# Kernel optimization log

Measured on AMD Instinct MI355X. Metric: run time of the kernel, lower is better.

Reference implementation:

```python
import jax, jax.numpy as jnp
import numpy as np

B, T, SEG = 64, 16, 50          # batch, n segments, segment length (cap 50 in original)
E, D, H, F = 512, 512, 8, 2048  # dim_embeddings, dim_encoder, n_heads, dim_ff
DH = D // H
SCALE = float(1.0 / np.sqrt(DH))


def _ln(x, g, b):
    m = jnp.mean(x, -1, keepdims=True)
    v = jnp.var(x, -1, keepdims=True)
    return (x - m) * jax.lax.rsqrt(v + 1e-5) * g + b


def _mha(q_in, kv_in, Wq, Wk, Wv, Wo, kv_lens):
    b, sq, _ = q_in.shape
    sk = kv_in.shape[1]
    q = (q_in @ Wq).reshape(b, sq, H, DH)
    k = (kv_in @ Wk).reshape(b, sk, H, DH)
    v = (kv_in @ Wv).reshape(b, sk, H, DH)
    scores = jnp.einsum('bqhd,bkhd->bhqk', q, k) * SCALE
    mask = jnp.arange(sk)[None, :] < kv_lens[:, None]  # [b, sk] key-padding mask
    scores = jnp.where(mask[:, None, None, :], scores, -1e9)
    a = jax.nn.softmax(scores, axis=-1)
    o = jnp.einsum('bhqk,bkhd->bqhd', a, v).reshape(b, sq, D)
    return o @ Wo


def _ffn(x, W1, W2):
    return jax.nn.relu(x @ W1) @ W2


def _encoder(x, lens, p):
    # TransformerEncoder: project E->D, masked self-attn + FFN, post-LN residuals
    h = x @ p['eWin']
    h = _ln(h + _mha(h, h, p['eWq'], p['eWk'], p['eWv'], p['eWo'], lens), p['eG1'], p['eB1'])
    return _ln(h + _ffn(h, p['eF1'], p['eF2']), p['eG2'], p['eB2'])


def _connection(prev, curr, prev_lens, p):
    # Connection: curr cross-attends over prev (masked by prev_lens) + FFN
    h = _ln(curr + _mha(curr, prev, p['cWq'], p['cWk'], p['cWv'], p['cWo'], prev_lens), p['cG1'], p['cB1'])
    return _ln(h + _ffn(h, p['cF1'], p['cF2']), p['cG2'], p['cB2'])


def _forward(seqs, ends, p):
    first_lens = jnp.minimum(ends[:, 0], SEG)
    encoded = _encoder(seqs[:, :SEG], first_lens, p)  # [B, SEG, D]
    # regular segmentation: ends[b,t] = (t+1)*SEG, so every step uses a full segment
    segs = seqs.reshape(B, T, SEG, E).transpose(1, 0, 2, 3)[1:]        # [T-1, B, SEG, E]
    seg_lens = jnp.minimum(ends[:, 1:] - ends[:, :-1], SEG).T          # [T-1, B]
    prev_lens = jnp.full((B,), SEG, jnp.int32)

    def step(enc, xs):
        seg, lens = xs
        currs = _encoder(seg, lens, p)
        out = _connection(enc, currs, prev_lens, p)
        return out, None  # out[-SEG:] == out since seq_len = min(diff, 50) = SEG

    encoded, _ = jax.lax.scan(step, encoded, (segs, seg_lens))
    return encoded


def setup_inputs():
    key = jax.random.key(0)
    ks = jax.random.split(key, 16)
    g = lambda k, s: jax.random.normal(k, s, jnp.float32) * 0.02
    inp = {
        'seqs': jax.random.normal(ks[0], (B, T * SEG, E), jnp.float32),
        'ends': jnp.broadcast_to((jnp.arange(1, T + 1) * SEG).astype(jnp.int32), (B, T)),
        'eWin': g(ks[1], (E, D)),
        'eWq': g(ks[2], (D, D)), 'eWk': g(ks[3], (D, D)),
        'eWv': g(ks[4], (D, D)), 'eWo': g(ks[5], (D, D)),
        'eG1': jnp.ones(D), 'eB1': jnp.zeros(D),
        'eF1': g(ks[6], (D, F)), 'eF2': g(ks[7], (F, D)),
        'eG2': jnp.ones(D), 'eB2': jnp.zeros(D),
        'cWq': g(ks[8], (D, D)), 'cWk': g(ks[9], (D, D)),
        'cWv': g(ks[10], (D, D)), 'cWo': g(ks[11], (D, D)),
        'cG1': jnp.ones(D), 'cB1': jnp.zeros(D),
        'cF1': g(ks[12], (D, F)), 'cF2': g(ks[13], (F, D)),
        'cG2': jnp.ones(D), 'cB2': jnp.zeros(D),
    }
    return inp


def reference(seqs, ends, eWin, eWq, eWk, eWv, eWo, eG1, eB1, eF1, eF2, eG2, eB2,
              cWq, cWk, cWv, cWo, cG1, cB1, cF1, cF2, cG2, cB2):
    p = dict(eWin=eWin, eWq=eWq, eWk=eWk, eWv=eWv, eWo=eWo, eG1=eG1, eB1=eB1,
             eF1=eF1, eF2=eF2, eG2=eG2, eB2=eB2, cWq=cWq, cWk=cWk, cWv=cWv,
             cWo=cWo, cG1=cG1, cB1=cB1, cF1=cF1, cF2=cF2, cG2=cG2, cB2=cB2)
    return _forward(seqs, ends, p)
```

## Files before the change

### kernel.cpp

```cpp
#include <hip/hip_runtime.h>


#define NB   64
#define NT   16
#define SEGL 50
#define DMODEL 512
#define DFF  2048
#define NHEAD 8
#define DHEAD 64

typedef unsigned short ushort_t;
typedef __attribute__((ext_vector_type(8))) short bfrag;
typedef __attribute__((ext_vector_type(4))) float ffrag;

__device__ __forceinline__ ushort_t f2b(float x) {
    union { float f; unsigned u; } c; c.f = x;
    unsigned r = c.u + 0x7fffu + ((c.u >> 16) & 1u);
    return (ushort_t)(r >> 16);
}

#define GLOAD_LDS16(g, l) __builtin_amdgcn_global_load_lds( \
    (const __attribute__((address_space(1))) void*)(g),      \
    (__attribute__((address_space(3))) void*)(l), 16, 0, 0)

template<int BM, int BN, int WROWS, int WCOLS>
__global__ __launch_bounds__(256) void mfma_gemm(
    const ushort_t* __restrict__ A, int agrp, long long astride,
    const ushort_t* __restrict__ Bt, ushort_t* __restrict__ C,
    int M, int N, int K, int relu)
{
    constexpr int WM = BM / WROWS, WN = BN / WCOLS;
    constexpr int SM = WM / 16, SN = WN / 16;
    constexpr int NSUBA = BM / 16, NSUBB = BN / 16;
    constexpr int NSUB = NSUBA + NSUBB;
    constexpr int NINST = NSUB * 2;
    constexpr int IPW = NINST / 4;
    constexpr int BUFS = NSUB * 1024;
    constexpr int EST = WN + 8;
    constexpr int LDS_KLOOP = 2 * BUFS;
    constexpr int LDS_EPI   = 4 * WM * EST;
    constexpr int LDS_SZ = LDS_KLOOP > LDS_EPI ? LDS_KLOOP : LDS_EPI;
    __shared__ ushort_t lds[LDS_SZ];

    const int tid = threadIdx.x;
    const int wave = tid >> 6, lane = tid & 63;
    const int wrow = wave / WCOLS, wcol = wave % WCOLS;
    const int bm = blockIdx.y * BM, bn = blockIdx.x * BN;
    const int lm = lane & 15, lq = lane >> 4;

    ffrag acc[SM][SN];
#pragma unroll
    for (int i = 0; i < SM; ++i)
#pragma unroll
        for (int j = 0; j < SN; ++j) acc[i][j] = (ffrag){0.f, 0.f, 0.f, 0.f};

    const ushort_t* gptr[IPW];
    int loff[IPW];
#pragma unroll
    for (int e = 0; e < IPW; ++e) {
        int g = wave * IPW + e;
        int s = g >> 1, h = g & 1;
        if (s < NSUBA) {
            int m = bm + s * 16 + lm;
            gptr[e] = A + (long long)(m / agrp) * astride
                        + (long long)(m % agrp) * K + h * 32 + lq * 8;
        } else {
            int n = bn + (s - NSUBA) * 16 + lm;
            gptr[e] = Bt + (long long)n * K + h * 32 + lq * 8;
        }
        loff[e] = s * 1024 + h * 512;
    }

#pragma unroll
    for (int e = 0; e < IPW; ++e)
        GLOAD_LDS16(gptr[e], &lds[loff[e]]);

    const int nk = K >> 6;
    for (int kk = 0; kk < nk; ++kk) {
        __syncthreads();
        if (kk + 1 < nk) {
            const int koff = (kk + 1) << 6;
            const int nb = (kk + 1) & 1;
#pragma unroll
            for (int e = 0; e < IPW; ++e)
                GLOAD_LDS16(gptr[e] + koff, &lds[nb * BUFS + loff[e]]);
        }
        const ushort_t* lb = &lds[(kk & 1) * BUFS];
#pragma unroll
        for (int h = 0; h < 2; ++h) {
            bfrag af[SM], bfg[SN];
#pragma unroll
            for (int i = 0; i < SM; ++i)
                af[i] = *(const bfrag*)&lb[(wrow * SM + i) * 1024 + h * 512 + lane * 8];
#pragma unroll
            for (int j = 0; j < SN; ++j)
                bfg[j] = *(const bfrag*)&lb[(NSUBA + wcol * SN + j) * 1024 + h * 512 + lane * 8];
#pragma unroll
            for (int i = 0; i < SM; ++i)
#pragma unroll
                for (int j = 0; j < SN; ++j)
                    acc[i][j] = __builtin_amdgcn_mfma_f32_16x16x32_bf16(
                        af[i], bfg[j], acc[i][j], 0, 0, 0);
        }
    }

    __syncthreads();
    ushort_t* ep = &lds[wave * WM * EST];
#pragma unroll
    for (int i = 0; i < SM; ++i)
#pragma unroll
        for (int j = 0; j < SN; ++j)
#pragma unroll
            for (int r = 0; r < 4; ++r) {
                int row = i * 16 + lq * 4 + r;
                int col = j * 16 + lm;
                float v = acc[i][j][r];
                if (relu) v = fmaxf(v, 0.f);
                ep[row * EST + col] = f2b(v);
            }
    constexpr int CPR = WN / 8;
    constexpr int RPI = 64 / CPR;
    const int lrow = lane / CPR, lcol = (lane % CPR) * 8;
#pragma unroll
    for (int it = 0; it < WM / RPI; ++it) {
        int row = it * RPI + lrow;
        uint4 v = *(const uint4*)&ep[row * EST + lcol];
        long long grow = bm + wrow * WM + row;
        int gcol = bn + wcol * WN + lcol;
        *(uint4*)&C[grow * N + gcol] = v;
    }
}

__global__ __launch_bounds__(256) void wtrans_k(
    const float* __restrict__ W, ushort_t* __restrict__ Wt, int K, int N)
{
    __shared__ float t[32][33];
    const int bk = blockIdx.y * 32, bn = blockIdx.x * 32;
    const int tx = threadIdx.x & 31, ty = threadIdx.x >> 5;
    for (int i = ty; i < 32; i += 8)
        t[i][tx] = W[(long long)(bk + i) * N + bn + tx];
    __syncthreads();
    for (int i = ty; i < 32; i += 8)
        Wt[(long long)(bn + i) * K + bk + tx] = f2b(t[tx][i]);
}

__global__ __launch_bounds__(256) void cvt_k(
    const float* __restrict__ in, ushort_t* __restrict__ out, long long n)
{
    long long i = ((long long)blockIdx.x * 256 + threadIdx.x) * 8;
    if (i >= n) return;
    float4 a = *(const float4*)(in + i);
    float4 b = *(const float4*)(in + i + 4);
    ushort_t o[8] = {f2b(a.x), f2b(a.y), f2b(a.z), f2b(a.w),
                     f2b(b.x), f2b(b.y), f2b(b.z), f2b(b.w)};
    *(uint4*)(out + i) = *(const uint4*)o;
}

__global__ __launch_bounds__(256) void attn_mfma_k(
    const ushort_t* __restrict__ Q, long long qns, long long qrs,
    const ushort_t* __restrict__ K, const ushort_t* __restrict__ V,
    long long kns, long long kvrs,
    ushort_t* __restrict__ O,
    const int* __restrict__ lens, int G, int t0)
{
    __shared__ ushort_t qs[64][72];
    __shared__ ushort_t ks[64][72];
    __shared__ ushort_t vt[64][72];
    const int n = blockIdx.x >> 3, h = blockIdx.x & 7;
    const int tid = threadIdx.x;
    const int wave = tid >> 6, lane = tid & 63;
    const int lm = lane & 15, lq = lane >> 4;
    int len = SEGL;
    if (lens) {
        int b = n / G, t = t0 + (n % G);
        len = lens[b * NT + t];
        if (len > SEGL) len = SEGL;
    }
    {
        uint4 z = {0, 0, 0, 0};
        uint4* vz = (uint4*)&vt[0][0];
        for (int i = tid; i < 64 * 72 / 8; i += 256) vz[i] = z;
    }
    __syncthreads();
    for (int idx = tid; idx < SEGL * 8; idx += 256) {
        int s = idx >> 3, d8 = (idx & 7) << 3;
        const ushort_t* qp = Q + (long long)n * qns + (long long)s * qrs + h * DHEAD + d8;
        const ushort_t* kp = K + (long long)n * kns + (long long)s * kvrs + h * DHEAD + d8;
        const ushort_t* vp = V + (long long)n * kns + (long long)s * kvrs + h * DHEAD + d8;
        *(uint4*)&qs[s][d8] = *(const uint4*)qp;
        *(uint4*)&ks[s][d8] = *(const uint4*)kp;
        uint4 v4 = *(const uint4*)vp;
        const ushort_t* vv = (const ushort_t*)&v4;
#pragma unroll
        for (int u = 0; u < 8; ++u) vt[d8 + u][s] = vv[u];
    }
    __syncthreads();

    ffrag sc[4];
#pragma unroll
    for (int nt = 0; nt < 4; ++nt) sc[nt] = (ffrag){0.f, 0.f, 0.f, 0.f};
#pragma unroll
    for (int kt = 0; kt < 2; ++kt) {
        bfrag a = *(const bfrag*)&qs[wave * 16 + lm][kt * 32 + lq * 8];
#pragma unroll
        for (int nt = 0; nt < 4; ++nt) {
            bfrag b = *(const bfrag*)&ks[nt * 16 + lm][kt * 32 + lq * 8];
            sc[nt] = __builtin_amdgcn_mfma_f32_16x16x32_bf16(a, b, sc[nt], 0, 0, 0);
        }
    }
    __syncthreads();

#pragma unroll
    for (int r = 0; r < 4; ++r) {
        float x[4];
        float mx = -1e30f;
#pragma unroll
        for (int nt = 0; nt < 4; ++nt) {
            int col = nt * 16 + lm;
            x[nt] = (col < len) ? sc[nt][r] * 0.125f : -1e9f;
            mx = fmaxf(mx, x[nt]);
        }
        for (int off = 8; off; off >>= 1) mx = fmaxf(mx, __shfl_xor(mx, off));
        float e[4], se = 0.f;
#pragma unroll
        for (int nt = 0; nt < 4; ++nt) { e[nt] = __expf(x[nt] - mx); se += e[nt]; }
        for (int off = 8; off; off >>= 1) se += __shfl_xor(se, off);
        float inv = 1.f / se;
        int row = wave * 16 + lq * 4 + r;
#pragma unroll
        for (int nt = 0; nt < 4; ++nt)
            qs[row][nt * 16 + lm] = f2b(e[nt] * inv);
    }
    __syncthreads();

    ffrag oc[4];
#pragma unroll
    for (int dt = 0; dt < 4; ++dt) oc[dt] = (ffrag){0.f, 0.f, 0.f, 0.f};
#pragma unroll
    for (int kt = 0; kt < 2; ++kt) {
        bfrag a = *(const bfrag*)&qs[wave * 16 + lm][kt * 32 + lq * 8];
#pragma unroll
        for (int dt = 0; dt < 4; ++dt) {
            bfrag b = *(const bfrag*)&vt[dt * 16 + lm][kt * 32 + lq * 8];
            oc[dt] = __builtin_amdgcn_mfma_f32_16x16x32_bf16(a, b, oc[dt], 0, 0, 0);
        }
    }
#pragma unroll
    for (int r = 0; r < 4; ++r) {
        int i = wave * 16 + lq * 4 + r;
        if (i < SEGL) {
            ushort_t* op = O + (long long)(n * SEGL + i) * DMODEL + h * DHEAD + lm;
#pragma unroll
            for (int dt = 0; dt < 4; ++dt)
                op[dt * 16] = f2b(oc[dt][r]);
        }
    }
}

__global__ __launch_bounds__(256) void cross_attn_k(
    const ushort_t* __restrict__ Qp, long long qns, long long qrs,
    const ushort_t* __restrict__ Prev, int pgrp, long long pstride,
    const ushort_t* __restrict__ Wkv,
    ushort_t* __restrict__ O)
{
    __shared__ ushort_t xp[64 * 264];
    __shared__ ushort_t qs[64][72];
    const int n = blockIdx.x >> 3, h = blockIdx.x & 7;
    const int tid = threadIdx.x;
    const int wave = tid >> 6, lane = tid & 63;
    const int lm = lane & 15, lq = lane >> 4;

    for (int idx = tid; idx < SEGL * 8; idx += 256) {
        int s = idx >> 3, d8 = (idx & 7) << 3;
        *(uint4*)&qs[s][d8] =
            *(const uint4*)(Qp + (long long)n * qns + (long long)s * qrs + h * DHEAD + d8);
    }

    const ushort_t* wbase = Wkv +
        (long long)((wave >> 1) * 512 + h * 64 + (wave & 1) * 32) * 512;
    ffrag kv[4][2];
#pragma unroll
    for (int i = 0; i < 4; ++i)
#pragma unroll
        for (int j = 0; j < 2; ++j) kv[i][j] = (ffrag){0.f, 0.f, 0.f, 0.f};

#pragma unroll
    for (int half = 0; half < 2; ++half) {
        __syncthreads();
        for (int idx = tid; idx < 64 * 33; idx += 256) {
            int s = idx / 33, c8 = (idx % 33) * 8;
            uint4 v = {0, 0, 0, 0};
            if (s < SEGL && c8 < 256) {
                long long r = (long long)n * SEGL + s;
                v = *(const uint4*)(Prev + (r / pgrp) * pstride
                                    + (r % pgrp) * DMODEL + half * 256 + c8);
            }
            *(uint4*)&xp[s * 264 + c8] = v;
        }
        __syncthreads();
#pragma unroll
        for (int k8 = 0; k8 < 8; ++k8) {
            const int kg = half * 256 + k8 * 32;
            bfrag bf[2], af[4];
#pragma unroll
            for (int j = 0; j < 2; ++j)
                bf[j] = *(const bfrag*)(wbase + (long long)(j * 16 + lm) * 512 + kg + lq * 8);
#pragma unroll
            for (int i = 0; i < 4; ++i)
                af[i] = *(const bfrag*)&xp[(i * 16 + lm) * 264 + k8 * 32 + lq * 8];
#pragma unroll
            for (int i = 0; i < 4; ++i)
#pragma unroll
                for (int j = 0; j < 2; ++j)
                    kv[i][j] = __builtin_amdgcn_mfma_f32_16x16x32_bf16(
                        af[i], bf[j], kv[i][j], 0, 0, 0);
        }
    }
    __syncthreads();
    ushort_t (*ks)[72] = (ushort_t(*)[72])&xp[0];
    ushort_t (*vt)[72] = (ushort_t(*)[72])&xp[64 * 72];
#pragma unroll
    for (int i = 0; i < 4; ++i)
#pragma unroll
        for (int j = 0; j < 2; ++j)
#pragma unroll
            for (int r = 0; r < 4; ++r) {
                int rowk = i * 16 + lq * 4 + r;
                int d = (wave & 1) * 32 + j * 16 + lm;
                ushort_t val = f2b(kv[i][j][r]);
                if (wave < 2) ks[rowk][d] = val;
                else          vt[d][rowk] = val;
            }
    __syncthreads();

    ffrag sc[4];
#pragma unroll
    for (int nt = 0; nt < 4; ++nt) sc[nt] = (ffrag){0.f, 0.f, 0.f, 0.f};
#pragma unroll
    for (int kt = 0; kt < 2; ++kt) {
        bfrag a = *(const bfrag*)&qs[wave * 16 + lm][kt * 32 + lq * 8];
#pragma unroll
        for (int nt = 0; nt < 4; ++nt) {
            bfrag b = *(const bfrag*)&ks[nt * 16 + lm][kt * 32 + lq * 8];
            sc[nt] = __builtin_amdgcn_mfma_f32_16x16x32_bf16(a, b, sc[nt], 0, 0, 0);
        }
    }
    __syncthreads();

#pragma unroll
    for (int r = 0; r < 4; ++r) {
        float x[4];
        float mx = -1e30f;
#pragma unroll
        for (int nt = 0; nt < 4; ++nt) {
            int col = nt * 16 + lm;
            x[nt] = (col < SEGL) ? sc[nt][r] * 0.125f : -1e9f;
            mx = fmaxf(mx, x[nt]);
        }
        for (int off = 8; off; off >>= 1) mx = fmaxf(mx, __shfl_xor(mx, off));
        float e[4], se = 0.f;
#pragma unroll
        for (int nt = 0; nt < 4; ++nt) { e[nt] = __expf(x[nt] - mx); se += e[nt]; }
        for (int off = 8; off; off >>= 1) se += __shfl_xor(se, off);
        float inv = 1.f / se;
        int row = wave * 16 + lq * 4 + r;
#pragma unroll
        for (int nt = 0; nt < 4; ++nt)
            qs[row][nt * 16 + lm] = f2b(e[nt] * inv);
    }
    __syncthreads();

    ffrag oc[4];
#pragma unroll
    for (int dt = 0; dt < 4; ++dt) oc[dt] = (ffrag){0.f, 0.f, 0.f, 0.f};
#pragma unroll
    for (int kt = 0; kt < 2; ++kt) {
        bfrag a = *(const bfrag*)&qs[wave * 16 + lm][kt * 32 + lq * 8];
#pragma unroll
        for (int dt = 0; dt < 4; ++dt) {
            bfrag b = *(const bfrag*)&vt[dt * 16 + lm][kt * 32 + lq * 8];
            oc[dt] = __builtin_amdgcn_mfma_f32_16x16x32_bf16(a, b, oc[dt], 0, 0, 0);
        }
    }
#pragma unroll
    for (int r = 0; r < 4; ++r) {
        int i = wave * 16 + lq * 4 + r;
        if (i < SEGL) {
            ushort_t* op = O + (long long)(n * SEGL + i) * DMODEL + h * DHEAD + lm;
#pragma unroll
            for (int dt = 0; dt < 4; ++dt)
                op[dt * 16] = f2b(oc[dt][r]);
        }
    }
}

template<bool OUTF32>
__global__ __launch_bounds__(256) void add_ln_k(
    const ushort_t* __restrict__ A, int agrp, long long astride,
    const ushort_t* __restrict__ Bv,
    const float* __restrict__ gamma, const float* __restrict__ beta,
    void* __restrict__ O, int ogrp, long long ostride, int M)
{
    const int wave = threadIdx.x >> 6, lane = threadIdx.x & 63;
    const int r = blockIdx.x * 4 + wave;
    if (r >= M) return;
    const ushort_t* a = A + (long long)(r / agrp) * astride + (long long)(r % agrp) * DMODEL;
    const ushort_t* b = Bv + (long long)r * DMODEL;
    float x[8];
    {
        uint4 a4 = *(const uint4*)(a + lane * 8);
        uint4 b4 = *(const uint4*)(b + lane * 8);
        const unsigned* aa = (const unsigned*)&a4;
        const unsigned* bb = (const unsigned*)&b4;
#pragma unroll
        for (int c = 0; c < 4; ++c) {
            union { unsigned u; float f; } alo, ahi, blo, bhi;
            alo.u = aa[c] << 16; ahi.u = aa[c] & 0xffff0000u;
            blo.u = bb[c] << 16; bhi.u = bb[c] & 0xffff0000u;
            x[2 * c]     = alo.f + blo.f;
            x[2 * c + 1] = ahi.f + bhi.f;
        }
    }
    float s = 0.f, s2 = 0.f;
#pragma unroll
    for (int i = 0; i < 8; ++i) { s += x[i]; s2 = fmaf(x[i], x[i], s2); }
    for (int off = 32; off; off >>= 1) {
        s += __shfl_xor(s, off);
        s2 += __shfl_xor(s2, off);
    }
    const float mean = s * (1.f / DMODEL);
    const float var = s2 * (1.f / DMODEL) - mean * mean;
    const float inv = rsqrtf(var + 1e-5f);
    float4 g0 = *(const float4*)(gamma + lane * 8);
    float4 g1 = *(const float4*)(gamma + lane * 8 + 4);
    float4 be0 = *(const float4*)(beta + lane * 8);
    float4 be1 = *(const float4*)(beta + lane * 8 + 4);
    float y[8];
    y[0] = (x[0] - mean) * inv * g0.x + be0.x;
    y[1] = (x[1] - mean) * inv * g0.y + be0.y;
    y[2] = (x[2] - mean) * inv * g0.z + be0.z;
    y[3] = (x[3] - mean) * inv * g0.w + be0.w;
    y[4] = (x[4] - mean) * inv * g1.x + be1.x;
    y[5] = (x[5] - mean) * inv * g1.y + be1.y;
    y[6] = (x[6] - mean) * inv * g1.z + be1.z;
    y[7] = (x[7] - mean) * inv * g1.w + be1.w;
    if (OUTF32) {
        float* o = (float*)O + (long long)(r / ogrp) * ostride + (long long)(r % ogrp) * DMODEL;
        *(float4*)(o + lane * 8) = *(float4*)&y[0];
        *(float4*)(o + lane * 8 + 4) = *(float4*)&y[4];
    } else {
        ushort_t* o = (ushort_t*)O + (long long)(r / ogrp) * ostride + (long long)(r % ogrp) * DMODEL;
        ushort_t ob[8];
#pragma unroll
        for (int i = 0; i < 8; ++i) ob[i] = f2b(y[i]);
        *(uint4*)(o + lane * 8) = *(const uint4*)ob;
    }
}

__global__ void lens_k(const int* __restrict__ ends, int* __restrict__ lens)
{
    int i = blockIdx.x * 256 + threadIdx.x;
    if (i >= NB * NT) return;
    int t = i & (NT - 1);
    int prev = t ? ends[i - 1] : 0;
    int l = ends[i] - prev;
    if (l > SEGL) l = SEGL;
    lens[i] = l;
}

extern "C" void kernel_launch(void* const* d_in, const int* in_sizes, int n_in,
                              void* d_out, int out_size, void* d_ws, size_t ws_size,
                              hipStream_t stream)
{
    const float* seqs = (const float*)d_in[0];
    const int*   ends = (const int*)d_in[1];
    const float* eG1 = (const float*)d_in[7],  *eB1 = (const float*)d_in[8];
    const float* eG2 = (const float*)d_in[11], *eB2 = (const float*)d_in[12];
    const float* cG1 = (const float*)d_in[17], *cB1 = (const float*)d_in[18];
    const float* cG2 = (const float*)d_in[21], *cB2 = (const float*)d_in[22];
    float* out = (float*)d_out;

    const int G = (ws_size >= (size_t)470000000) ? 8 : 4;
    const long long CH = 1638400LL * G;

    ushort_t* ws = (ushort_t*)d_ws;
    const long long SEQROW = (long long)NT * SEGL * DMODEL;
    ushort_t* SEQB = ws;
    ushort_t* WT   = SEQB + 26214400LL;
    ushort_t* ENC  = WT   + 6553600LL;
    ushort_t* BUF0 = ENC  + 26214400LL;
    ushort_t* QKV  = BUF0 + CH;
    ushort_t* BUF4 = QKV  + 3 * CH;
    ushort_t* BUF1 = BUF4 + CH;
    ushort_t* BUF2 = BUF1 + CH;
    ushort_t* MID  = BUF2 + CH;
    ushort_t* OUTB = MID  + 4 * CH;
    ushort_t* QALL = OUTB + 1638400LL;
    int*      lens = (int*)(QALL + 24576000LL);

    const ushort_t* eWinT = WT + 0;
    const ushort_t* WQKVe = WT + 262144;
    const ushort_t* eWoT  = WT + 1048576;
    const ushort_t* eF1T  = WT + 1310720;
    const ushort_t* eF2T  = WT + 2359296;
    const ushort_t* cWqT  = WT + 3407872;
    const ushort_t* cKV   = WT + 3670016;
    const ushort_t* cWoT  = WT + 4194304;
    const ushort_t* cF1T  = WT + 4456448;
    const ushort_t* cF2T  = WT + 5505024;

    struct WMap { int src; long long dst; int K, N; };
    const WMap wm[13] = {
        {2,  0,       512, 512},
        {3,  262144,  512, 512},
        {4,  524288,  512, 512},
        {5,  786432,  512, 512},
        {6,  1048576, 512, 512},
        {9,  1310720, 512, 2048},
        {10, 2359296, 2048, 512},
        {13, 3407872, 512, 512},
        {14, 3670016, 512, 512},
        {15, 3932160, 512, 512},
        {16, 4194304, 512, 512},
        {19, 4456448, 512, 2048},
        {20, 5505024, 2048, 512},
    };

    cvt_k<<<12800, 256, 0, stream>>>(seqs, SEQB, 26214400LL);
    for (int w = 0; w < 13; ++w) {
        dim3 g(wm[w].N / 32, wm[w].K / 32);
        wtrans_k<<<g, 256, 0, stream>>>((const float*)d_in[wm[w].src],
                                        WT + wm[w].dst, wm[w].K, wm[w].N);
    }
    lens_k<<<4, 256, 0, stream>>>(ends, lens);

    auto gemmL = [&](const ushort_t* A, int agrp, long long astr, const ushort_t* Bt,
                     ushort_t* C, int M, int N, int K, int relu) {
        dim3 g(N / 128, M / 128);
        mfma_gemm<128, 128, 2, 2><<<g, 256, 0, stream>>>(A, agrp, astr, Bt, C, M, N, K, relu);
    };
    auto gemmS = [&](const ushort_t* A, int agrp, long long astr, const ushort_t* Bt,
                     ushort_t* C, int M, int N, int K, int relu) {
        dim3 g(N / 64, M / 64);
        mfma_gemm<64, 64, 2, 2><<<g, 256, 0, stream>>>(A, agrp, astr, Bt, C, M, N, K, relu);
    };

    const int Mc = NB * G * SEGL;
    for (int c = 0; c < NT / G; ++c) {
        const int t0 = c * G;
        const ushort_t* Abase = SEQB + (long long)t0 * SEGL * DMODEL;
        ushort_t* ENCc = ENC + (long long)t0 * SEGL * DMODEL;
        gemmL(Abase, G * SEGL, SEQROW, eWinT, BUF0, Mc, 512, 512, 0);
        gemmL(BUF0, Mc, 0, WQKVe, QKV, Mc, 1536, 512, 0);
        attn_mfma_k<<<NB * G * NHEAD, 256, 0, stream>>>(
            QKV, 50LL * 1536, 1536, QKV + 512, QKV + 1024, 50LL * 1536, 1536,
            BUF4, lens, G, t0);
        gemmL(BUF4, Mc, 0, eWoT, BUF1, Mc, 512, 512, 0);
        add_ln_k<false><<<Mc / 4, 256, 0, stream>>>(BUF0, Mc, 0, BUF1, eG1, eB1,
                                                    BUF2, Mc, 0, Mc);
        gemmL(BUF2, Mc, 0, eF1T, MID, Mc, 2048, 512, 1);
        gemmL(MID, Mc, 0, eF2T, BUF1, Mc, 512, 2048, 0);
        add_ln_k<false><<<Mc / 4, 256, 0, stream>>>(BUF2, Mc, 0, BUF1, eG2, eB2,
                                                    ENCc, G * SEGL, SEQROW, Mc);
    }

    gemmL(ENC + 25600, 750, SEQROW, cWqT, QALL, 48000, 512, 512, 0);

    const int Ms = NB * SEGL;
    for (int t = 1; t < NT; ++t) {
        const ushort_t* currA = ENC + (long long)t * SEGL * DMODEL;
        const ushort_t* prevA; int pg; long long ps;
        if (t == 1) { prevA = ENC;  pg = SEGL; ps = SEQROW; }
        else        { prevA = OUTB; pg = Ms;   ps = 0; }
        cross_attn_k<<<NB * NHEAD, 256, 0, stream>>>(
            QALL + (long long)(t - 1) * 25600, 750LL * 512, 512,
            prevA, pg, ps, cKV, BUF4);
        gemmS(BUF4, Ms, 0, cWoT, BUF0, Ms, 512, 512, 0);
        add_ln_k<false><<<Ms / 4, 256, 0, stream>>>(currA, SEGL, SEQROW, BUF0, cG1, cB1,
                                                    BUF2, Ms, 0, Ms);
        gemmS(BUF2, Ms, 0, cF1T, MID, Ms, 2048, 512, 1);
        gemmS(MID, Ms, 0, cF2T, BUF0, Ms, 512, 2048, 0);
        if (t == NT - 1)
            add_ln_k<true><<<Ms / 4, 256, 0, stream>>>(BUF2, Ms, 0, BUF0, cG2, cB2,
                                                       out, Ms, 0, Ms);
        else
            add_ln_k<false><<<Ms / 4, 256, 0, stream>>>(BUF2, Ms, 0, BUF0, cG2, cB2,
                                                        OUTB, Ms, 0, Ms);
    }
}
```

Before: 2.770 ms.

## Fuse sequential cross-attention phase into one persistent per-batch kernel

Replaces the 15-step host loop of cross_attn/Wo GEMM/LN/FFN GEMMs/LN launches with a single persistent kernel, phase2_seq. It launches 64 blocks of 1024 threads, one per batch element, and each block loops over all timesteps with the previous output kept in LDS and intermediates in a per-block global scratch. The aim is to remove roughly 100 small kernel launches and the inter-kernel round trips. In exchange it uses only 64 workgroups on a GPU with many more CUs, and each block recomputes K/V and streams all the weights from L2 on every step, so compute parallelism is low.

```diff
diff --git a/kernel.cpp b/kernel.cpp
--- a/kernel.cpp
+++ b/kernel.cpp
@@ -22,6 +22,8 @@
 #define GLOAD_LDS16(g, l) __builtin_amdgcn_global_load_lds( \
     (const __attribute__((address_space(1))) void*)(g),      \
     (__attribute__((address_space(3))) void*)(l), 16, 0, 0)
+
+#define MFMA16(a, b, c) __builtin_amdgcn_mfma_f32_16x16x32_bf16(a, b, c, 0, 0, 0)
 
 template<int BM, int BN, int WROWS, int WCOLS>
 __global__ __launch_bounds__(256) void mfma_gemm(
@@ -99,8 +101,7 @@
             for (int i = 0; i < SM; ++i)
 #pragma unroll
                 for (int j = 0; j < SN; ++j)
-                    acc[i][j] = __builtin_amdgcn_mfma_f32_16x16x32_bf16(
-                        af[i], bfg[j], acc[i][j], 0, 0, 0);
+                    acc[i][j] = MFMA16(af[i], bfg[j], acc[i][j]);
         }
     }
 
@@ -205,7 +206,7 @@
 #pragma unroll
         for (int nt = 0; nt < 4; ++nt) {
             bfrag b = *(const bfrag*)&ks[nt * 16 + lm][kt * 32 + lq * 8];
-            sc[nt] = __builtin_amdgcn_mfma_f32_16x16x32_bf16(a, b, sc[nt], 0, 0, 0);
+            sc[nt] = MFMA16(a, b, sc[nt]);
         }
     }
     __syncthreads();
@@ -242,144 +243,7 @@
 #pragma unroll
         for (int dt = 0; dt < 4; ++dt) {
             bfrag b = *(const bfrag*)&vt[dt * 16 + lm][kt * 32 + lq * 8];
-            oc[dt] = __builtin_amdgcn_mfma_f32_16x16x32_bf16(a, b, oc[dt], 0, 0, 0);
-        }
-    }
-#pragma unroll
-    for (int r = 0; r < 4; ++r) {
-        int i = wave * 16 + lq * 4 + r;
-        if (i < SEGL) {
-            ushort_t* op = O + (long long)(n * SEGL + i) * DMODEL + h * DHEAD + lm;
-#pragma unroll
-            for (int dt = 0; dt < 4; ++dt)
-                op[dt * 16] = f2b(oc[dt][r]);
-        }
-    }
-}
-
-__global__ __launch_bounds__(256) void cross_attn_k(
-    const ushort_t* __restrict__ Qp, long long qns, long long qrs,
-    const ushort_t* __restrict__ Prev, int pgrp, long long pstride,
-    const ushort_t* __restrict__ Wkv,
-    ushort_t* __restrict__ O)
-{
-    __shared__ ushort_t xp[64 * 264];
-    __shared__ ushort_t qs[64][72];
-    const int n = blockIdx.x >> 3, h = blockIdx.x & 7;
-    const int tid = threadIdx.x;
-    const int wave = tid >> 6, lane = tid & 63;
-    const int lm = lane & 15, lq = lane >> 4;
-
-    for (int idx = tid; idx < SEGL * 8; idx += 256) {
-        int s = idx >> 3, d8 = (idx & 7) << 3;
-        *(uint4*)&qs[s][d8] =
-            *(const uint4*)(Qp + (long long)n * qns + (long long)s * qrs + h * DHEAD + d8);
-    }
-
-    const ushort_t* wbase = Wkv +
-        (long long)((wave >> 1) * 512 + h * 64 + (wave & 1) * 32) * 512;
-    ffrag kv[4][2];
-#pragma unroll
-    for (int i = 0; i < 4; ++i)
-#pragma unroll
-        for (int j = 0; j < 2; ++j) kv[i][j] = (ffrag){0.f, 0.f, 0.f, 0.f};
-
-#pragma unroll
-    for (int half = 0; half < 2; ++half) {
-        __syncthreads();
-        for (int idx = tid; idx < 64 * 33; idx += 256) {
-            int s = idx / 33, c8 = (idx % 33) * 8;
-            uint4 v = {0, 0, 0, 0};
-            if (s < SEGL && c8 < 256) {
-                long long r = (long long)n * SEGL + s;
-                v = *(const uint4*)(Prev + (r / pgrp) * pstride
-                                    + (r % pgrp) * DMODEL + half * 256 + c8);
-            }
-            *(uint4*)&xp[s * 264 + c8] = v;
-        }
-        __syncthreads();
-#pragma unroll
-        for (int k8 = 0; k8 < 8; ++k8) {
-            const int kg = half * 256 + k8 * 32;
-            bfrag bf[2], af[4];
-#pragma unroll
-            for (int j = 0; j < 2; ++j)
-                bf[j] = *(const bfrag*)(wbase + (long long)(j * 16 + lm) * 512 + kg + lq * 8);
-#pragma unroll
-            for (int i = 0; i < 4; ++i)
-                af[i] = *(const bfrag*)&xp[(i * 16 + lm) * 264 + k8 * 32 + lq * 8];
-#pragma unroll
-            for (int i = 0; i < 4; ++i)
-#pragma unroll
-                for (int j = 0; j < 2; ++j)
-                    kv[i][j] = __builtin_amdgcn_mfma_f32_16x16x32_bf16(
-                        af[i], bf[j], kv[i][j], 0, 0, 0);
-        }
-    }
-    __syncthreads();
-    ushort_t (*ks)[72] = (ushort_t(*)[72])&xp[0];
-    ushort_t (*vt)[72] = (ushort_t(*)[72])&xp[64 * 72];
-#pragma unroll
-    for (int i = 0; i < 4; ++i)
-#pragma unroll
-        for (int j = 0; j < 2; ++j)
-#pragma unroll
-            for (int r = 0; r < 4; ++r) {
-                int rowk = i * 16 + lq * 4 + r;
-                int d = (wave & 1) * 32 + j * 16 + lm;
-                ushort_t val = f2b(kv[i][j][r]);
-                if (wave < 2) ks[rowk][d] = val;
-                else          vt[d][rowk] = val;
-            }
-    __syncthreads();
-
-    ffrag sc[4];
-#pragma unroll
-    for (int nt = 0; nt < 4; ++nt) sc[nt] = (ffrag){0.f, 0.f, 0.f, 0.f};
-#pragma unroll
-    for (int kt = 0; kt < 2; ++kt) {
-        bfrag a = *(const bfrag*)&qs[wave * 16 + lm][kt * 32 + lq * 8];
-#pragma unroll
-        for (int nt = 0; nt < 4; ++nt) {
-            bfrag b = *(const bfrag*)&ks[nt * 16 + lm][kt * 32 + lq * 8];
-            sc[nt] = __builtin_amdgcn_mfma_f32_16x16x32_bf16(a, b, sc[nt], 0, 0, 0);
-        }
-    }
-    __syncthreads();
-
-#pragma unroll
-    for (int r = 0; r < 4; ++r) {
-        float x[4];
-        float mx = -1e30f;
-#pragma unroll
-        for (int nt = 0; nt < 4; ++nt) {
-            int col = nt * 16 + lm;
-            x[nt] = (col < SEGL) ? sc[nt][r] * 0.125f : -1e9f;
-            mx = fmaxf(mx, x[nt]);
-        }
-        for (int off = 8; off; off >>= 1) mx = fmaxf(mx, __shfl_xor(mx, off));
-        float e[4], se = 0.f;
-#pragma unroll
-        for (int nt = 0; nt < 4; ++nt) { e[nt] = __expf(x[nt] - mx); se += e[nt]; }
-        for (int off = 8; off; off >>= 1) se += __shfl_xor(se, off);
-        float inv = 1.f / se;
-        int row = wave * 16 + lq * 4 + r;
-#pragma unroll
-        for (int nt = 0; nt < 4; ++nt)
-            qs[row][nt * 16 + lm] = f2b(e[nt] * inv);
-    }
-    __syncthreads();
-
-    ffrag oc[4];
-#pragma unroll
-    for (int dt = 0; dt < 4; ++dt) oc[dt] = (ffrag){0.f, 0.f, 0.f, 0.f};
-#pragma unroll
-    for (int kt = 0; kt < 2; ++kt) {
-        bfrag a = *(const bfrag*)&qs[wave * 16 + lm][kt * 32 + lq * 8];
-#pragma unroll
-        for (int dt = 0; dt < 4; ++dt) {
-            bfrag b = *(const bfrag*)&vt[dt * 16 + lm][kt * 32 + lq * 8];
-            oc[dt] = __builtin_amdgcn_mfma_f32_16x16x32_bf16(a, b, oc[dt], 0, 0, 0);
+            oc[dt] = MFMA16(a, b, oc[dt]);
         }
     }
 #pragma unroll
@@ -468,6 +332,338 @@
     lens[i] = l;
 }
 
+__global__ __launch_bounds__(1024) void phase2_seq(
+    const ushort_t* __restrict__ ENC, const ushort_t* __restrict__ QALL,
+    const ushort_t* __restrict__ Wkv, const ushort_t* __restrict__ WoT,
+    const ushort_t* __restrict__ F1T, const ushort_t* __restrict__ F2T,
+    const float* __restrict__ G1v, const float* __restrict__ B1v,
+    const float* __restrict__ G2v, const float* __restrict__ B2v,
+    ushort_t* __restrict__ SCR, float* __restrict__ out)
+{
+    extern __shared__ ushort_t lds[];
+    ushort_t* Pb = lds;
+    ushort_t* Mb = lds + 64 * 520;
+    const int n = blockIdx.x;
+    const int tid = threadIdx.x;
+    const int w = tid >> 6, lane = tid & 63;
+    const int lm = lane & 15, lq = lane >> 4;
+    const int hh = w >> 1, wp = w & 1;
+
+    ushort_t* Kg  = SCR + (long long)n * 163840;
+    ushort_t* VTg = Kg + 32768;
+    ushort_t* Sg  = Kg + 65536;
+    ushort_t* ATg = Kg + 98304;
+    ushort_t* Hg  = Kg + 131072;
+
+    {
+        uint4 z = {0, 0, 0, 0};
+        for (int i = tid; i < 64 * 520 / 8; i += 1024) ((uint4*)Pb)[i] = z;
+    }
+    __syncthreads();
+    for (int idx = tid; idx < 50 * 64; idx += 1024) {
+        int s = idx >> 6, c8 = (idx & 63) << 3;
+        *(uint4*)&Pb[s * 520 + c8] =
+            *(const uint4*)(ENC + (long long)n * 409600 + (long long)s * 512 + c8);
+    }
+    __syncthreads();
+
+#pragma unroll 1
+    for (int t = 1; t < NT; ++t) {
+        const ushort_t* Qb = QALL + (long long)n * 384000 + (long long)(t - 1) * 25600;
+
+        {
+            ffrag ka[4][2], va[4][2];
+#pragma unroll
+            for (int i = 0; i < 4; ++i)
+#pragma unroll
+                for (int j = 0; j < 2; ++j) {
+                    ka[i][j] = (ffrag){0.f, 0.f, 0.f, 0.f};
+                    va[i][j] = (ffrag){0.f, 0.f, 0.f, 0.f};
+                }
+            const ushort_t* wk = Wkv + (long long)(w * 32) * 512;
+            const ushort_t* wv = Wkv + (long long)(512 + w * 32) * 512;
+#pragma unroll
+            for (int k8 = 0; k8 < 16; ++k8) {
+                bfrag af[4];
+#pragma unroll
+                for (int i = 0; i < 4; ++i)
+                    af[i] = *(const bfrag*)&Pb[(i * 16 + lm) * 520 + k8 * 32 + lq * 8];
+#pragma unroll
+                for (int j = 0; j < 2; ++j) {
+                    bfrag bk = *(const bfrag*)(wk + (long long)(j * 16 + lm) * 512 + k8 * 32 + lq * 8);
+                    bfrag bv = *(const bfrag*)(wv + (long long)(j * 16 + lm) * 512 + k8 * 32 + lq * 8);
+#pragma unroll
+                    for (int i = 0; i < 4; ++i) {
+                        ka[i][j] = MFMA16(af[i], bk, ka[i][j]);
+                        va[i][j] = MFMA16(af[i], bv, va[i][j]);
+                    }
+                }
+            }
+#pragma unroll
+            for (int i = 0; i < 4; ++i)
+#pragma unroll
+                for (int j = 0; j < 2; ++j)
+#pragma unroll
+                    for (int r = 0; r < 4; ++r) {
+                        int row = i * 16 + lq * 4 + r;
+                        int col = w * 32 + j * 16 + lm;
+                        Kg[row * 512 + col] = f2b(ka[i][j][r]);
+                        VTg[col * 64 + row] = f2b(va[i][j][r]);
+                    }
+        }
+        __syncthreads();
+
+        {
+            ffrag sc[2][4];
+#pragma unroll
+            for (int i = 0; i < 2; ++i)
+#pragma unroll
+                for (int j = 0; j < 4; ++j) sc[i][j] = (ffrag){0.f, 0.f, 0.f, 0.f};
+#pragma unroll
+            for (int kk = 0; kk < 2; ++kk) {
+                bfrag aq[2];
+#pragma unroll
+                for (int ii = 0; ii < 2; ++ii)
+                    aq[ii] = *(const bfrag*)(Qb + (long long)((wp * 2 + ii) * 16 + lm) * 512
+                                             + hh * 64 + kk * 32 + lq * 8);
+#pragma unroll
+                for (int j = 0; j < 4; ++j) {
+                    bfrag bk = *(const bfrag*)&Kg[(j * 16 + lm) * 512 + hh * 64 + kk * 32 + lq * 8];
+#pragma unroll
+                    for (int ii = 0; ii < 2; ++ii)
+                        sc[ii][j] = MFMA16(aq[ii], bk, sc[ii][j]);
+                }
+            }
+#pragma unroll
+            for (int ii = 0; ii < 2; ++ii)
+#pragma unroll
+                for (int r = 0; r < 4; ++r) {
+                    float x[4], mx = -1e30f;
+#pragma unroll
+                    for (int j = 0; j < 4; ++j) {
+                        int col = j * 16 + lm;
+                        x[j] = (col < SEGL) ? sc[ii][j][r] * 0.125f : -1e9f;
+                        mx = fmaxf(mx, x[j]);
+                    }
+                    for (int off = 8; off; off >>= 1) mx = fmaxf(mx, __shfl_xor(mx, off));
+                    float e[4], se = 0.f;
+#pragma unroll
+                    for (int j = 0; j < 4; ++j) { e[j] = __expf(x[j] - mx); se += e[j]; }
+                    for (int off = 8; off; off >>= 1) se += __shfl_xor(se, off);
+                    float inv = 1.f / se;
+                    int row = (wp * 2 + ii) * 16 + lq * 4 + r;
+#pragma unroll
+                    for (int j = 0; j < 4; ++j)
+                        Sg[hh * 4096 + row * 64 + j * 16 + lm] = f2b(e[j] * inv);
+                }
+        }
+        __syncthreads();
+
+        {
+            ffrag oc[2][4];
+#pragma unroll
+            for (int i = 0; i < 2; ++i)
+#pragma unroll
+                for (int j = 0; j < 4; ++j) oc[i][j] = (ffrag){0.f, 0.f, 0.f, 0.f};
+#pragma unroll
+            for (int kk = 0; kk < 2; ++kk) {
+                bfrag as[2];
+#pragma unroll
+                for (int ii = 0; ii < 2; ++ii)
+                    as[ii] = *(const bfrag*)&Sg[hh * 4096 + ((wp * 2 + ii) * 16 + lm) * 64
+                                                + kk * 32 + lq * 8];
+#pragma unroll
+                for (int j = 0; j < 4; ++j) {
+                    bfrag bv = *(const bfrag*)&VTg[(hh * 64 + j * 16 + lm) * 64 + kk * 32 + lq * 8];
+#pragma unroll
+                    for (int ii = 0; ii < 2; ++ii)
+                        oc[ii][j] = MFMA16(as[ii], bv, oc[ii][j]);
+                }
+            }
+#pragma unroll
+            for (int ii = 0; ii < 2; ++ii)
+#pragma unroll
+                for (int j = 0; j < 4; ++j)
+#pragma unroll
+                    for (int r = 0; r < 4; ++r) {
+                        int row = (wp * 2 + ii) * 16 + lq * 4 + r;
+                        int col = hh * 64 + j * 16 + lm;
+                        ATg[row * 512 + col] = f2b(oc[ii][j][r]);
+                    }
+        }
+        __syncthreads();
+
+        {
+            ffrag acc[4][2];
+#pragma unroll
+            for (int i = 0; i < 4; ++i)
+#pragma unroll
+                for (int j = 0; j < 2; ++j) acc[i][j] = (ffrag){0.f, 0.f, 0.f, 0.f};
+#pragma unroll
+            for (int k8 = 0; k8 < 16; ++k8) {
+                bfrag af[4];
+#pragma unroll
+                for (int i = 0; i < 4; ++i)
+                    af[i] = *(const bfrag*)&ATg[(i * 16 + lm) * 512 + k8 * 32 + lq * 8];
+#pragma unroll
+                for (int j = 0; j < 2; ++j) {
+                    bfrag bw = *(const bfrag*)(WoT + (long long)(w * 32 + j * 16 + lm) * 512
+                                               + k8 * 32 + lq * 8);
+#pragma unroll
+                    for (int i = 0; i < 4; ++i)
+                        acc[i][j] = MFMA16(af[i], bw, acc[i][j]);
+                }
+            }
+#pragma unroll
+            for (int i = 0; i < 4; ++i)
+#pragma unroll
+                for (int j = 0; j < 2; ++j)
+#pragma unroll
+                    for (int r = 0; r < 4; ++r)
+                        Hg[(i * 16 + lq * 4 + r) * 512 + w * 32 + j * 16 + lm] = f2b(acc[i][j][r]);
+        }
+        __syncthreads();
+
+        for (int r = w; r < SEGL; r += 16) {
+            const ushort_t* cr = ENC + (long long)n * 409600 + (long long)(t * 50 + r) * 512;
+            uint4 a4 = *(const uint4*)&Hg[r * 512 + lane * 8];
+            uint4 b4 = *(const uint4*)(cr + lane * 8);
+            const unsigned* aa = (const unsigned*)&a4;
+            const unsigned* bb = (const unsigned*)&b4;
+            float x[8];
+#pragma unroll
+            for (int c = 0; c < 4; ++c) {
+                union { unsigned u; float f; } alo, ahi, blo, bhi;
+                alo.u = aa[c] << 16; ahi.u = aa[c] & 0xffff0000u;
+                blo.u = bb[c] << 16; bhi.u = bb[c] & 0xffff0000u;
+                x[2 * c]     = alo.f + blo.f;
+                x[2 * c + 1] = ahi.f + bhi.f;
+            }
+            float s = 0.f, s2 = 0.f;
+#pragma unroll
+            for (int i = 0; i < 8; ++i) { s += x[i]; s2 = fmaf(x[i], x[i], s2); }
+            for (int off = 32; off; off >>= 1) { s += __shfl_xor(s, off); s2 += __shfl_xor(s2, off); }
+            float mean = s * (1.f / DMODEL);
+            float var = s2 * (1.f / DMODEL) - mean * mean;
+            float inv = rsqrtf(var + 1e-5f);
+            float4 g0 = *(const float4*)(G1v + lane * 8);
+            float4 g1 = *(const float4*)(G1v + lane * 8 + 4);
+            float4 e0 = *(const float4*)(B1v + lane * 8);
+            float4 e1 = *(const float4*)(B1v + lane * 8 + 4);
+            ushort_t ob[8];
+            ob[0] = f2b((x[0] - mean) * inv * g0.x + e0.x);
+            ob[1] = f2b((x[1] - mean) * inv * g0.y + e0.y);
+            ob[2] = f2b((x[2] - mean) * inv * g0.z + e0.z);
+            ob[3] = f2b((x[3] - mean) * inv * g0.w + e0.w);
+            ob[4] = f2b((x[4] - mean) * inv * g1.x + e1.x);
+            ob[5] = f2b((x[5] - mean) * inv * g1.y + e1.y);
+            ob[6] = f2b((x[6] - mean) * inv * g1.z + e1.z);
+            ob[7] = f2b((x[7] - mean) * inv * g1.w + e1.w);
+            *(uint4*)&Hg[r * 512 + lane * 8] = *(const uint4*)ob;
+        }
+        __syncthreads();
+
+        ffrag fa[4][2];
+#pragma unroll
+        for (int i = 0; i < 4; ++i)
+#pragma unroll
+            for (int j = 0; j < 2; ++j) fa[i][j] = (ffrag){0.f, 0.f, 0.f, 0.f};
+#pragma unroll 1
+        for (int cc = 0; cc < 8; ++cc) {
+            ffrag m1[4];
+#pragma unroll
+            for (int i = 0; i < 4; ++i) m1[i] = (ffrag){0.f, 0.f, 0.f, 0.f};
+#pragma unroll
+            for (int k8 = 0; k8 < 16; ++k8) {
+                bfrag ah[4];
+#pragma unroll
+                for (int i = 0; i < 4; ++i)
+                    ah[i] = *(const bfrag*)&Hg[(i * 16 + lm) * 512 + k8 * 32 + lq * 8];
+                bfrag b1 = *(const bfrag*)(F1T + (long long)(cc * 256 + w * 16 + lm) * 512
+                                           + k8 * 32 + lq * 8);
+#pragma unroll
+                for (int i = 0; i < 4; ++i) m1[i] = MFMA16(ah[i], b1, m1[i]);
+            }
+            __syncthreads();
+#pragma unroll
+            for (int i = 0; i < 4; ++i)
+#pragma unroll
+                for (int r = 0; r < 4; ++r)
+                    Mb[(i * 16 + lq * 4 + r) * 264 + w * 16 + lm] = f2b(fmaxf(m1[i][r], 0.f));
+            __syncthreads();
+#pragma unroll
+            for (int k8 = 0; k8 < 8; ++k8) {
+                bfrag am[4];
+#pragma unroll
+                for (int i = 0; i < 4; ++i)
+                    am[i] = *(const bfrag*)&Mb[(i * 16 + lm) * 264 + k8 * 32 + lq * 8];
+#pragma unroll
+                for (int j = 0; j < 2; ++j) {
+                    bfrag b2 = *(const bfrag*)(F2T + (long long)(w * 32 + j * 16 + lm) * 2048
+                                               + cc * 256 + k8 * 32 + lq * 8);
+#pragma unroll
+                    for (int i = 0; i < 4; ++i) fa[i][j] = MFMA16(am[i], b2, fa[i][j]);
+                }
+            }
+        }
+#pragma unroll
+        for (int i = 0; i < 4; ++i)
+#pragma unroll
+            for (int j = 0; j < 2; ++j)
+#pragma unroll
+                for (int r = 0; r < 4; ++r)
+                    ATg[(i * 16 + lq * 4 + r) * 512 + w * 32 + j * 16 + lm] = f2b(fa[i][j][r]);
+        __syncthreads();
+
+        for (int r = w; r < SEGL; r += 16) {
+            uint4 a4 = *(const uint4*)&Hg[r * 512 + lane * 8];
+            uint4 b4 = *(const uint4*)&ATg[r * 512 + lane * 8];
+            const unsigned* aa = (const unsigned*)&a4;
+            const unsigned* bb = (const unsigned*)&b4;
+            float x[8];
+#pragma unroll
+            for (int c = 0; c < 4; ++c) {
+                union { unsigned u; float f; } alo, ahi, blo, bhi;
+                alo.u = aa[c] << 16; ahi.u = aa[c] & 0xffff0000u;
+                blo.u = bb[c] << 16; bhi.u = bb[c] & 0xffff0000u;
+                x[2 * c]     = alo.f + blo.f;
+                x[2 * c + 1] = ahi.f + bhi.f;
+            }
+            float s = 0.f, s2 = 0.f;
+#pragma unroll
+            for (int i = 0; i < 8; ++i) { s += x[i]; s2 = fmaf(x[i], x[i], s2); }
+            for (int off = 32; off; off >>= 1) { s += __shfl_xor(s, off); s2 += __shfl_xor(s2, off); }
+            float mean = s * (1.f / DMODEL);
+            float var = s2 * (1.f / DMODEL) - mean * mean;
+            float inv = rsqrtf(var + 1e-5f);
+            float4 g0 = *(const float4*)(G2v + lane * 8);
+            float4 g1 = *(const float4*)(G2v + lane * 8 + 4);
+            float4 e0 = *(const float4*)(B2v + lane * 8);
+            float4 e1 = *(const float4*)(B2v + lane * 8 + 4);
+            float y[8];
+            y[0] = (x[0] - mean) * inv * g0.x + e0.x;
+            y[1] = (x[1] - mean) * inv * g0.y + e0.y;
+            y[2] = (x[2] - mean) * inv * g0.z + e0.z;
+            y[3] = (x[3] - mean) * inv * g0.w + e0.w;
+            y[4] = (x[4] - mean) * inv * g1.x + e1.x;
+            y[5] = (x[5] - mean) * inv * g1.y + e1.y;
+            y[6] = (x[6] - mean) * inv * g1.z + e1.z;
+            y[7] = (x[7] - mean) * inv * g1.w + e1.w;
+            if (t == NT - 1) {
+                float* o = out + ((long long)n * 50 + r) * 512 + lane * 8;
+                *(float4*)o = *(float4*)&y[0];
+                *(float4*)(o + 4) = *(float4*)&y[4];
+            } else {
+                ushort_t ob[8];
+#pragma unroll
+                for (int i = 0; i < 8; ++i) ob[i] = f2b(y[i]);
+                *(uint4*)&Pb[r * 520 + lane * 8] = *(const uint4*)ob;
+            }
+        }
+        __syncthreads();
+    }
+}
+
 extern "C" void kernel_launch(void* const* d_in, const int* in_sizes, int n_in,
                               void* d_out, int out_size, void* d_ws, size_t ws_size,
                               hipStream_t stream)
@@ -538,11 +734,6 @@
                      ushort_t* C, int M, int N, int K, int relu) {
         dim3 g(N / 128, M / 128);
         mfma_gemm<128, 128, 2, 2><<<g, 256, 0, stream>>>(A, agrp, astr, Bt, C, M, N, K, relu);
-    };
-    auto gemmS = [&](const ushort_t* A, int agrp, long long astr, const ushort_t* Bt,
-                     ushort_t* C, int M, int N, int K, int relu) {
-        dim3 g(N / 64, M / 64);
-        mfma_gemm<64, 64, 2, 2><<<g, 256, 0, stream>>>(A, agrp, astr, Bt, C, M, N, K, relu);
     };
 
     const int Mc = NB * G * SEGL;
@@ -566,25 +757,17 @@
 
     gemmL(ENC + 25600, 750, SEQROW, cWqT, QALL, 48000, 512, 512, 0);
 
-    const int Ms = NB * SEGL;
-    for (int t = 1; t < NT; ++t) {
-        const ushort_t* currA = ENC + (long long)t * SEGL * DMODEL;
-        const ushort_t* prevA; int pg; long long ps;
-        if (t == 1) { prevA = ENC;  pg = SEGL; ps = SEQROW; }
-        else        { prevA = OUTB; pg = Ms;   ps = 0; }
-        cross_attn_k<<<NB * NHEAD, 256, 0, stream>>>(
-            QALL + (long long)(t - 1) * 25600, 750LL * 512, 512,
-            prevA, pg, ps, cKV, BUF4);
-        gemmS(BUF4, Ms, 0, cWoT, BUF0, Ms, 512, 512, 0);
-        add_ln_k<false><<<Ms / 4, 256, 0, stream>>>(currA, SEGL, SEQROW, BUF0, cG1, cB1,
-                                                    BUF2, Ms, 0, Ms);
-        gemmS(BUF2, Ms, 0, cF1T, MID, Ms, 2048, 512, 1);
-        gemmS(MID, Ms, 0, cF2T, BUF0, Ms, 512, 2048, 0);
-        if (t == NT - 1)
-            add_ln_k<true><<<Ms / 4, 256, 0, stream>>>(BUF2, Ms, 0, BUF0, cG2, cB2,
-                                                       out, Ms, 0, Ms);
-        else
-            add_ln_k<false><<<Ms / 4, 256, 0, stream>>>(BUF2, Ms, 0, BUF0, cG2, cB2,
-                                                        OUTB, Ms, 0, Ms);
-    }
-}
+    {
+        constexpr int LDS_BYTES = (64 * 520 + 64 * 264) * 2;
+        static bool attr_set = false;
+        if (!attr_set) {
+            hipFuncSetAttribute((const void*)phase2_seq,
+                                hipFuncAttributeMaxDynamicSharedMemorySize,
+                                LDS_BYTES);
+            attr_set = true;
+        }
+        phase2_seq<<<64, 1024, LDS_BYTES, stream>>>(
+            ENC, QALL, cKV, cWoT, cF1T, cF2T,
+            cG1, cB1, cG2, cB2, MID, out);
+    }
+}
```

Result: slower. 10.77 ms (+288.8%).

## Fuse connection-stage GEMMs with residual add and LayerNorm in one kernel

Applied to the files above, without the earlier changes.

Adds a gemm_ln_k kernel in which each 512-thread block computes a full 64x512 output row tile, then does the residual add and LayerNorm in its epilogue. It replaces the Wo GEMM plus add_ln and the FF2 GEMM plus add_ln pairs in the sequential connection loop. This removes two launches per step and the round trip of the intermediate through global memory. In exchange, the grid shrinks to Ms/64 = 50 blocks, so most CUs sit idle and per-block work grows, especially for the K=2048 FF2 GEMM.

```diff
diff --git a/kernel.cpp b/kernel.cpp
--- a/kernel.cpp
+++ b/kernel.cpp
@@ -22,6 +22,8 @@
 #define GLOAD_LDS16(g, l) __builtin_amdgcn_global_load_lds( \
     (const __attribute__((address_space(1))) void*)(g),      \
     (__attribute__((address_space(3))) void*)(l), 16, 0, 0)
+
+#define MFMA16(a, b, c) __builtin_amdgcn_mfma_f32_16x16x32_bf16(a, b, c, 0, 0, 0)
 
 template<int BM, int BN, int WROWS, int WCOLS>
 __global__ __launch_bounds__(256) void mfma_gemm(
@@ -99,8 +101,7 @@
             for (int i = 0; i < SM; ++i)
 #pragma unroll
                 for (int j = 0; j < SN; ++j)
-                    acc[i][j] = __builtin_amdgcn_mfma_f32_16x16x32_bf16(
-                        af[i], bfg[j], acc[i][j], 0, 0, 0);
+                    acc[i][j] = MFMA16(af[i], bfg[j], acc[i][j]);
         }
     }
 
@@ -128,6 +129,146 @@
         long long grow = bm + wrow * WM + row;
         int gcol = bn + wcol * WN + lcol;
         *(uint4*)&C[grow * N + gcol] = v;
+    }
+}
+
+template<bool OUTF32>
+__global__ __launch_bounds__(512, 2) void gemm_ln_k(
+    const ushort_t* __restrict__ A, int agrp, long long astride,
+    const ushort_t* __restrict__ Bt, int K,
+    const ushort_t* __restrict__ Res, int rgrp, long long rstride,
+    const float* __restrict__ gamma, const float* __restrict__ beta,
+    void* __restrict__ O)
+{
+    constexpr int NSUBA = 4, NSUBB = 32, NSUB = 36;
+    constexpr int IPW = NSUB * 2 / 8;
+    constexpr int BUFS = NSUB * 1024;
+    extern __shared__ ushort_t lds[];
+
+    const int tid = threadIdx.x;
+    const int wave = tid >> 6, lane = tid & 63;
+    const int bm = blockIdx.x * 64;
+    const int lm = lane & 15, lq = lane >> 4;
+
+    ffrag acc[4][4];
+#pragma unroll
+    for (int i = 0; i < 4; ++i)
+#pragma unroll
+        for (int j = 0; j < 4; ++j) acc[i][j] = (ffrag){0.f, 0.f, 0.f, 0.f};
+
+    const ushort_t* gptr[IPW];
+    int loff[IPW];
+#pragma unroll
+    for (int e = 0; e < IPW; ++e) {
+        int g = wave * IPW + e;
+        int s = g >> 1, h = g & 1;
+        if (s < NSUBA) {
+            int m = bm + s * 16 + lm;
+            gptr[e] = A + (long long)(m / agrp) * astride
+                        + (long long)(m % agrp) * K + h * 32 + lq * 8;
+        } else {
+            int n = (s - NSUBA) * 16 + lm;
+            gptr[e] = Bt + (long long)n * K + h * 32 + lq * 8;
+        }
+        loff[e] = s * 1024 + h * 512;
+    }
+
+#pragma unroll
+    for (int e = 0; e < IPW; ++e)
+        GLOAD_LDS16(gptr[e], &lds[loff[e]]);
+
+    const int nk = K >> 6;
+    for (int kk = 0; kk < nk; ++kk) {
+        __syncthreads();
+        if (kk + 1 < nk) {
+            const int koff = (kk + 1) << 6;
+            const int nb = (kk + 1) & 1;
+#pragma unroll
+            for (int e = 0; e < IPW; ++e)
+                GLOAD_LDS16(gptr[e] + koff, &lds[nb * BUFS + loff[e]]);
+        }
+        const ushort_t* lb = &lds[(kk & 1) * BUFS];
+#pragma unroll
+        for (int h = 0; h < 2; ++h) {
+            bfrag af[4], bfg[4];
+#pragma unroll
+            for (int i = 0; i < 4; ++i)
+                af[i] = *(const bfrag*)&lb[i * 1024 + h * 512 + lane * 8];
+#pragma unroll
+            for (int j = 0; j < 4; ++j)
+                bfg[j] = *(const bfrag*)&lb[(NSUBA + wave * 4 + j) * 1024 + h * 512 + lane * 8];
+#pragma unroll
+            for (int i = 0; i < 4; ++i)
+#pragma unroll
+                for (int j = 0; j < 4; ++j)
+                    acc[i][j] = MFMA16(af[i], bfg[j], acc[i][j]);
+        }
+    }
+
+    __syncthreads();
+    ushort_t* Cs = lds;
+#pragma unroll
+    for (int i = 0; i < 4; ++i)
+#pragma unroll
+        for (int j = 0; j < 4; ++j)
+#pragma unroll
+            for (int r = 0; r < 4; ++r) {
+                int row = i * 16 + lq * 4 + r;
+                int col = wave * 64 + j * 16 + lm;
+                Cs[row * 520 + col] = f2b(acc[i][j][r]);
+            }
+    __syncthreads();
+
+    for (int r = wave; r < 64; r += 8) {
+        long long rr = bm + r;
+        const ushort_t* b = Res + (rr / rgrp) * rstride + (rr % rgrp) * DMODEL;
+        uint4 a4 = *(const uint4*)&Cs[r * 520 + lane * 8];
+        uint4 b4 = *(const uint4*)(b + lane * 8);
+        const unsigned* aa = (const unsigned*)&a4;
+        const unsigned* bb = (const unsigned*)&b4;
+        float x[8];
+#pragma unroll
+        for (int c = 0; c < 4; ++c) {
+            union { unsigned u; float f; } alo, ahi, blo, bhi;
+            alo.u = aa[c] << 16; ahi.u = aa[c] & 0xffff0000u;
+            blo.u = bb[c] << 16; bhi.u = bb[c] & 0xffff0000u;
+            x[2 * c]     = alo.f + blo.f;
+            x[2 * c + 1] = ahi.f + bhi.f;
+        }
+        float s = 0.f, s2 = 0.f;
+#pragma unroll
+        for (int i = 0; i < 8; ++i) { s += x[i]; s2 = fmaf(x[i], x[i], s2); }
+        for (int off = 32; off; off >>= 1) {
+            s += __shfl_xor(s, off);
+            s2 += __shfl_xor(s2, off);
+        }
+        const float mean = s * (1.f / DMODEL);
+        const float var = s2 * (1.f / DMODEL) - mean * mean;
+        const float inv = rsqrtf(var + 1e-5f);
+        float4 g0 = *(const float4*)(gamma + lane * 8);
+        float4 g1 = *(const float4*)(gamma + lane * 8 + 4);
+        float4 e0 = *(const float4*)(beta + lane * 8);
+        float4 e1 = *(const float4*)(beta + lane * 8 + 4);
+        float y[8];
+        y[0] = (x[0] - mean) * inv * g0.x + e0.x;
+        y[1] = (x[1] - mean) * inv * g0.y + e0.y;
+        y[2] = (x[2] - mean) * inv * g0.z + e0.z;
+        y[3] = (x[3] - mean) * inv * g0.w + e0.w;
+        y[4] = (x[4] - mean) * inv * g1.x + e1.x;
+        y[5] = (x[5] - mean) * inv * g1.y + e1.y;
+        y[6] = (x[6] - mean) * inv * g1.z + e1.z;
+        y[7] = (x[7] - mean) * inv * g1.w + e1.w;
+        if (OUTF32) {
+            float* o = (float*)O + rr * DMODEL + lane * 8;
+            *(float4*)o = *(float4*)&y[0];
+            *(float4*)(o + 4) = *(float4*)&y[4];
+        } else {
+            ushort_t* o = (ushort_t*)O + rr * DMODEL + lane * 8;
+            ushort_t ob[8];
+#pragma unroll
+            for (int i = 0; i < 8; ++i) ob[i] = f2b(y[i]);
+            *(uint4*)o = *(const uint4*)ob;
+        }
     }
 }
 
@@ -205,7 +346,7 @@
 #pragma unroll
         for (int nt = 0; nt < 4; ++nt) {
             bfrag b = *(const bfrag*)&ks[nt * 16 + lm][kt * 32 + lq * 8];
-            sc[nt] = __builtin_amdgcn_mfma_f32_16x16x32_bf16(a, b, sc[nt], 0, 0, 0);
+            sc[nt] = MFMA16(a, b, sc[nt]);
         }
     }
     __syncthreads();
@@ -242,7 +383,7 @@
 #pragma unroll
         for (int dt = 0; dt < 4; ++dt) {
             bfrag b = *(const bfrag*)&vt[dt * 16 + lm][kt * 32 + lq * 8];
-            oc[dt] = __builtin_amdgcn_mfma_f32_16x16x32_bf16(a, b, oc[dt], 0, 0, 0);
+            oc[dt] = MFMA16(a, b, oc[dt]);
         }
     }
 #pragma unroll
@@ -312,8 +453,7 @@
             for (int i = 0; i < 4; ++i)
 #pragma unroll
                 for (int j = 0; j < 2; ++j)
-                    kv[i][j] = __builtin_amdgcn_mfma_f32_16x16x32_bf16(
-                        af[i], bf[j], kv[i][j], 0, 0, 0);
+                    kv[i][j] = MFMA16(af[i], bf[j], kv[i][j]);
         }
     }
     __syncthreads();
@@ -342,7 +482,7 @@
 #pragma unroll
         for (int nt = 0; nt < 4; ++nt) {
             bfrag b = *(const bfrag*)&ks[nt * 16 + lm][kt * 32 + lq * 8];
-            sc[nt] = __builtin_amdgcn_mfma_f32_16x16x32_bf16(a, b, sc[nt], 0, 0, 0);
+            sc[nt] = MFMA16(a, b, sc[nt]);
         }
     }
     __syncthreads();
@@ -379,7 +519,7 @@
 #pragma unroll
         for (int dt = 0; dt < 4; ++dt) {
             bfrag b = *(const bfrag*)&vt[dt * 16 + lm][kt * 32 + lq * 8];
-            oc[dt] = __builtin_amdgcn_mfma_f32_16x16x32_bf16(a, b, oc[dt], 0, 0, 0);
+            oc[dt] = MFMA16(a, b, oc[dt]);
         }
     }
 #pragma unroll
@@ -545,6 +685,16 @@
         mfma_gemm<64, 64, 2, 2><<<g, 256, 0, stream>>>(A, agrp, astr, Bt, C, M, N, K, relu);
     };
 
+    constexpr int GLN_LDS = 2 * 36864 * 2;
+    static bool attr_set = false;
+    if (!attr_set) {
+        hipFuncSetAttribute((const void*)gemm_ln_k<false>,
+                            hipFuncAttributeMaxDynamicSharedMemorySize, GLN_LDS);
+        hipFuncSetAttribute((const void*)gemm_ln_k<true>,
+                            hipFuncAttributeMaxDynamicSharedMemorySize, GLN_LDS);
+        attr_set = true;
+    }
+
     const int Mc = NB * G * SEGL;
     for (int c = 0; c < NT / G; ++c) {
         const int t0 = c * G;
@@ -575,16 +725,14 @@
         cross_attn_k<<<NB * NHEAD, 256, 0, stream>>>(
             QALL + (long long)(t - 1) * 25600, 750LL * 512, 512,
             prevA, pg, ps, cKV, BUF4);
-        gemmS(BUF4, Ms, 0, cWoT, BUF0, Ms, 512, 512, 0);
-        add_ln_k<false><<<Ms / 4, 256, 0, stream>>>(currA, SEGL, SEQROW, BUF0, cG1, cB1,
-                                                    BUF2, Ms, 0, Ms);
+        gemm_ln_k<false><<<Ms / 64, 512, GLN_LDS, stream>>>(
+            BUF4, Ms, 0, cWoT, 512, currA, SEGL, SEQROW, cG1, cB1, BUF2);
         gemmS(BUF2, Ms, 0, cF1T, MID, Ms, 2048, 512, 1);
-        gemmS(MID, Ms, 0, cF2T, BUF0, Ms, 512, 2048, 0);
         if (t == NT - 1)
-            add_ln_k<true><<<Ms / 4, 256, 0, stream>>>(BUF2, Ms, 0, BUF0, cG2, cB2,
-                                                       out, Ms, 0, Ms);
+            gemm_ln_k<true><<<Ms / 64, 512, GLN_LDS, stream>>>(
+                MID, Ms, 0, cF2T, 2048, BUF2, Ms, 0, cG2, cB2, out);
         else
-            add_ln_k<false><<<Ms / 4, 256, 0, stream>>>(BUF2, Ms, 0, BUF0, cG2, cB2,
-                                                        OUTB, Ms, 0, Ms);
-    }
-}
+            gemm_ln_k<false><<<Ms / 64, 512, GLN_LDS, stream>>>(
+                MID, Ms, 0, cF2T, 2048, BUF2, Ms, 0, cG2, cB2, OUTB);
+    }
+}
```

Result: slower. 3.754 ms (+35.5%).
